# Kernel tuning notes

Hardware: AMD Instinct MI355X
Metric: run time of the kernel (lower is better)

## Reference

```python
import jax, jax.numpy as jnp
import numpy as np

ALPHA = 1.5
BETA = 45.0
LAMDA = 0.5
B = 8192   # batch_size
D = 128    # feature dim (hardcoded in original via zeros((1,128)))
V = 4      # number of views stacked in fj
EPS = 1e-12  # F.normalize eps


def _l2norm_rows(x):
    n = jnp.sqrt(jnp.sum(x * x, axis=-1, keepdims=True))
    return x / jnp.maximum(n, EPS)


def setup_inputs() -> dict:
    key = jax.random.key(0)
    k1, k2 = jax.random.split(key)
    fi = jax.random.normal(k1, (B, D), dtype=jnp.float32)
    fj = jax.random.normal(k2, (V, B, D), dtype=jnp.float32)
    # L2-normalize embeddings so exp(beta*(SVM - lamda)) stays finite (beta=45)
    fi = _l2norm_rows(fi)
    fj = _l2norm_rows(fj)
    return {"fi": fi, "fj": fj, "b": V}


def avg_svm(fi, fj):
    # Original: per-row softmax-weighted average of fj rows, renormalized,
    # dotted with fi row, averaged over the batch.
    A = fi @ fj.T                      # [B, B] pairwise logits
    W = jax.nn.softmax(A, axis=1)      # softmax over j (alphalist / sumofalpha)
    Vw = W @ fj                        # [B, D] softmax-weighted averages
    Vn = _l2norm_rows(Vw)              # F.normalize(p=2, dim=1)
    return jnp.mean(jnp.sum(fi * Vn, axis=1))  # mean_i fi[i] . Vn[i]


def reference(fi, fj, b):
    b = int(b)
    # SMM1 is recomputed identically every outer iteration in the original;
    # compute once and multiply the per-iteration term by (b-1).
    smm1 = avg_svm(fi, fi)
    if b > 2:
        # inner loop: SMM2sum is a running (cumulative) sum over j=1..b-2,
        # and exp(beta*(SMM2sum - lamda)) is added at every step.
        s_vals = jnp.stack([avg_svm(fi, fj[j]) for j in range(1, b - 1)])
        cum = jnp.cumsum(s_vals)
        ssum = jnp.sum(jnp.exp(BETA * (cum - LAMDA)))
    else:
        ssum = jnp.exp(BETA * (avg_svm(fi, fj) - LAMDA))
    term = (1.0 / ALPHA) * jnp.log1p(jnp.exp(-ALPHA * (smm1 - LAMDA))) \
         + (1.0 / BETA) * jnp.log1p(ssum)
    loss = (b - 1) * term
    return jnp.squeeze(loss)
```

## Files before the change

kernel.cpp:

```cpp
#include <hip/hip_runtime.h>

#define BDIM 8192
#define DDIM 128

typedef __attribute__((ext_vector_type(4))) float floatx4;
typedef __attribute__((ext_vector_type(4))) int   intx4;
typedef __attribute__((ext_vector_type(8))) int   intx8;
typedef long i64;

#define SLAB (BDIM * DDIM)
#define G8_OFF 64
#define G8T_OFF (64 + 3 * SLAB)

__device__ inline void load_lds16(const void* g, void* l) {
    __builtin_amdgcn_global_load_lds(
        (const __attribute__((address_space(1))) unsigned int*)g,
        (__attribute__((address_space(3))) unsigned int*)l, 16, 0, 0);
}

__device__ inline intx8 ld_pair(const char* base, int c0) {
    union { intx8 v; intx4 h[2]; } u;
    u.h[0] = *(const intx4*)(base + c0 * 16);
    u.h[1] = *(const intx4*)(base + (c0 ^ 1) * 16);
    return u.v;
}

__device__ inline float exp_fast(float x) {
    return __builtin_amdgcn_exp2f(x * 1.44269504088896341f);
}

__global__ __launch_bounds__(256)
void prep_kernel(const float* __restrict__ fi, const float* __restrict__ fj,
                 unsigned char* __restrict__ g8, unsigned char* __restrict__ g8T,
                 float* __restrict__ acc)
{
    const int p = blockIdx.y;
    const int kblock = blockIdx.x;
    const int rbase = kblock * 32;
    const int tid = threadIdx.x;
    if (p == 0 && kblock == 0 && tid < 8) acc[tid] = 0.f;
    const float* src = (p == 0) ? fi : (fj + (size_t)p * SLAB);

    __shared__ __align__(16) unsigned char T8[32][144];

    {
        const int row = tid >> 3, c = tid & 7;
        const float* sp = src + (size_t)(rbase + row) * DDIM + c * 16;
        float4 f0 = ((const float4*)sp)[0];
        float4 f1 = ((const float4*)sp)[1];
        float4 f2 = ((const float4*)sp)[2];
        float4 f3 = ((const float4*)sp)[3];
        alignas(16) int w[4];
        w[0] = __builtin_amdgcn_cvt_pk_fp8_f32(f0.x, f0.y, 0, false);
        w[0] = __builtin_amdgcn_cvt_pk_fp8_f32(f0.z, f0.w, w[0], true);
        w[1] = __builtin_amdgcn_cvt_pk_fp8_f32(f1.x, f1.y, 0, false);
        w[1] = __builtin_amdgcn_cvt_pk_fp8_f32(f1.z, f1.w, w[1], true);
        w[2] = __builtin_amdgcn_cvt_pk_fp8_f32(f2.x, f2.y, 0, false);
        w[2] = __builtin_amdgcn_cvt_pk_fp8_f32(f2.z, f2.w, w[2], true);
        w[3] = __builtin_amdgcn_cvt_pk_fp8_f32(f3.x, f3.y, 0, false);
        w[3] = __builtin_amdgcn_cvt_pk_fp8_f32(f3.z, f3.w, w[3], true);
        int4 v = *(int4*)w;
        *(int4*)(g8 + (size_t)p * SLAB + (size_t)(rbase + row) * DDIM + c * 16) = v;
        *(int4*)(&T8[row][c * 16]) = v;
    }
    __syncthreads();
    {
        const int d = tid >> 1, half = tid & 1;
        const int s = (d >> 2) & 3;
        alignas(16) unsigned char bb[16];
        #pragma unroll
        for (int x = 0; x < 16; ++x) {
            int g  = (half << 1) + (x >> 3);
            int u  = x & 7;
            int kl = ((g ^ s) << 2) + (u & 3) + ((u >> 2) << 4);
            bb[x] = T8[kl][d];
        }
        *(int4*)(g8T + (size_t)p * SLAB + (size_t)kblock * 4096 + d * 32 + half * 16) =
            *(int4*)bb;
    }
}

__global__ __launch_bounds__(256, 3)
void flash_kernel(const float* __restrict__ fi,
                  const unsigned char* __restrict__ g8,
                  const unsigned char* __restrict__ g8T,
                  float* __restrict__ acc)
{
    const int b = blockIdx.x;
    const int gp = (b & 7) * 96 + (b >> 3);
    const int p = gp >> 8;
    const int qbase = (gp & 255) * 32;
    const int tid = threadIdx.x;
    const int wave = tid >> 6, lane = tid & 63;
    const int quad = lane >> 4, col = lane & 15;

    __shared__ __align__(16) char smem[49792];
    #define KOFF 0
    #define VOFF 16384
    #define OOFF 32768
    #define PVOFF 49664

    const unsigned char* g8p  = g8  + (size_t)p * SLAB;
    const unsigned char* g8Tp = g8T + (size_t)p * SLAB;

    intx8 qf[2];
    #pragma unroll
    for (int qt = 0; qt < 2; ++qt) {
        const intx4* qp = (const intx4*)(g8 + (size_t)(qbase + qt * 16 + col) * DDIM +
                                         quad * 32);
        union { intx8 v; intx4 h[2]; } u;
        u.h[0] = qp[0];
        u.h[1] = qp[1];
        qf[qt] = u.v;
    }

    floatx4 O[2][8];
    #pragma unroll
    for (int qt = 0; qt < 2; ++qt)
        #pragma unroll
        for (int dt = 0; dt < 8; ++dt)
            O[qt][dt] = (floatx4){0.f, 0.f, 0.f, 0.f};

    const unsigned char* kSrc = g8p + (size_t)wave * 4096 +
        (size_t)(lane >> 3) * 128 + (size_t)(((lane & 7) ^ ((lane >> 3) & 7)) * 16);
    const unsigned char* vSrc = g8Tp + (size_t)wave * 4096 + (size_t)lane * 16;

    auto stage = [&]() {
        #pragma unroll
        for (int i = 0; i < 4; ++i)
            load_lds16(kSrc + i * 1024, smem + KOFF + wave * 4096 + i * 1024);
        #pragma unroll
        for (int i = 0; i < 4; ++i)
            load_lds16(vSrc + i * 1024, smem + VOFF + wave * 4096 + i * 1024);
        kSrc += 16384;
        vSrc += 16384;
    };

    const char* kb0 = smem + KOFF + wave * 4096 + col * 128;
    const char* kb1 = smem + KOFF + wave * 4096 + (16 + col) * 128;
    const int   kc  = (quad * 2) ^ (col & 7);
    const char* vbase = smem + VOFF + wave * 4096 + col * 32 +
                        ((quad ^ (col >> 2)) * 8);

    stage();

    for (int k = 0; k < 64; ++k) {
        asm volatile("s_waitcnt vmcnt(0)" ::: "memory");

        intx8 kf0 = ld_pair(kb0, kc);
        intx8 kf1 = ld_pair(kb1, kc);
        i64 vf[8];
        #pragma unroll
        for (int dt = 0; dt < 8; ++dt)
            vf[dt] = *(const i64*)(vbase + dt * 512);

        asm volatile("s_waitcnt lgkmcnt(0)" ::: "memory");
        if (k < 63) stage();

        floatx4 S[2][2];
        __builtin_amdgcn_s_setprio(1);
        S[0][0] = __builtin_amdgcn_mfma_scale_f32_16x16x128_f8f6f4(
            kf0, qf[0], (floatx4){0.f,0.f,0.f,0.f}, 0, 0, 0, 127, 0, 127);
        S[0][1] = __builtin_amdgcn_mfma_scale_f32_16x16x128_f8f6f4(
            kf0, qf[1], (floatx4){0.f,0.f,0.f,0.f}, 0, 0, 0, 127, 0, 127);
        S[1][0] = __builtin_amdgcn_mfma_scale_f32_16x16x128_f8f6f4(
            kf1, qf[0], (floatx4){0.f,0.f,0.f,0.f}, 0, 0, 0, 127, 0, 127);
        S[1][1] = __builtin_amdgcn_mfma_scale_f32_16x16x128_f8f6f4(
            kf1, qf[1], (floatx4){0.f,0.f,0.f,0.f}, 0, 0, 0, 127, 0, 127);
        __builtin_amdgcn_s_setprio(0);

        i64 pf[2];
        #pragma unroll
        for (int qt = 0; qt < 2; ++qt) {
            int w0 = __builtin_amdgcn_cvt_pk_fp8_f32(
                exp_fast(S[0][qt][0]), exp_fast(S[0][qt][1]), 0, false);
            w0 = __builtin_amdgcn_cvt_pk_fp8_f32(
                exp_fast(S[0][qt][2]), exp_fast(S[0][qt][3]), w0, true);
            int w1 = __builtin_amdgcn_cvt_pk_fp8_f32(
                exp_fast(S[1][qt][0]), exp_fast(S[1][qt][1]), 0, false);
            w1 = __builtin_amdgcn_cvt_pk_fp8_f32(
                exp_fast(S[1][qt][2]), exp_fast(S[1][qt][3]), w1, true);
            union { i64 l; int i[2]; } u;
            u.i[0] = w0;
            u.i[1] = w1;
            pf[qt] = u.l;
        }

        __builtin_amdgcn_s_setprio(1);
        #pragma unroll
        for (int qt = 0; qt < 2; ++qt)
            #pragma unroll
            for (int dt = 0; dt < 8; ++dt)
                O[qt][dt] = __builtin_amdgcn_mfma_f32_16x16x32_fp8_fp8(
                    pf[qt], vf[dt], O[qt][dt], 0, 0, 0);
        __builtin_amdgcn_s_setprio(0);
    }

    float* OL = (float*)(smem + OOFF);
    #pragma unroll 1
    for (int w = 0; w < 4; ++w) {
        if (wave == w) {
            #pragma unroll
            for (int qt = 0; qt < 2; ++qt)
                #pragma unroll
                for (int dt = 0; dt < 8; ++dt)
                    #pragma unroll
                    for (int r = 0; r < 4; ++r) {
                        const int q = qt * 16 + quad * 4 + r;
                        const int d = dt * 16 + col;
                        if (w == 0) OL[q * 132 + d]  = O[qt][dt][r];
                        else        OL[q * 132 + d] += O[qt][dt][r];
                    }
        }
        __syncthreads();
    }

    {
        const int q = tid >> 3, dc = (tid & 7) * 16;
        const float* fq = fi + (size_t)(qbase + q) * DDIM + dc;
        float dot = 0.f, nr = 0.f;
        #pragma unroll
        for (int u = 0; u < 16; ++u) {
            float o = OL[q * 132 + dc + u];
            dot += fq[u] * o;
            nr  += o * o;
        }
        #pragma unroll
        for (int m = 1; m < 8; m <<= 1) {
            dot += __shfl_xor(dot, m, 64);
            nr  += __shfl_xor(nr,  m, 64);
        }
        float* pv = (float*)(smem + PVOFF);
        if ((tid & 7) == 0)
            pv[q] = dot * rsqrtf(fmaxf(nr, 1e-30f));
        __syncthreads();
        if (tid < 32) {
            float val = pv[tid];
            #pragma unroll
            for (int m = 1; m < 32; m <<= 1) val += __shfl_xor(val, m, 64);
            if (tid == 0) atomicAdd(&acc[p], val);
        }
    }
}

__global__ void final_kernel(const float* __restrict__ acc, float* __restrict__ out)
{
    if (threadIdx.x == 0 && blockIdx.x == 0) {
        const double s0 = (double)acc[0] / (double)BDIM;
        const double s1 = (double)acc[1] / (double)BDIM;
        const double s2 = (double)acc[2] / (double)BDIM;
        const double t1 = (1.0 / 1.5) * log1p(exp(-1.5 * (s0 - 0.5)));
        const double ssum = exp(45.0 * (s1 - 0.5)) + exp(45.0 * (s1 + s2 - 0.5));
        const double t2 = (1.0 / 45.0) * log1p(ssum);
        out[0] = (float)(3.0 * (t1 + t2));
    }
}

extern "C" void kernel_launch(void* const* d_in, const int* in_sizes, int n_in,
                              void* d_out, int out_size, void* d_ws, size_t ws_size,
                              hipStream_t stream)
{
    const float* fi = (const float*)d_in[0];
    const float* fj = (const float*)d_in[1];

    float* acc = (float*)d_ws;
    unsigned char* g8  = (unsigned char*)d_ws + G8_OFF;
    unsigned char* g8T = (unsigned char*)d_ws + G8T_OFF;

    prep_kernel <<<dim3(BDIM / 32, 3), 256, 0, stream>>>(fi, fj, g8, g8T, acc);
    flash_kernel<<<dim3(768), 256, 0, stream>>>(fi, g8, g8T, acc);
    final_kernel<<<1, 64, 0, stream>>>(acc, (float*)d_out);
}
```

Measured before the change: 155.1 us.

## Batch four K tiles per PV step with K=128 fp8 MFMA and direct-global V loads

The PV product now accumulates P fragments from four consecutive key tiles into one 128-wide operand and issues the 16x16x128 scaled fp8 MFMA, cutting the PV MFMA count fourfold. V is read straight from global memory in a new transposed layout produced by the prep kernel, instead of being staged through LDS. This shrinks LDS use so more blocks can fit per CU. The cost is exposed global-load latency on the V fragments, which are no longer prefetched, and a different ordering of the transposed V data.

```diff
diff --git a/kernel.cpp b/kernel.cpp
--- a/kernel.cpp
+++ b/kernel.cpp
@@ -65,18 +65,23 @@
     }
     __syncthreads();
     {
-        const int d = tid >> 1, half = tid & 1;
-        const int s = (d >> 2) & 3;
-        alignas(16) unsigned char bb[16];
-        #pragma unroll
-        for (int x = 0; x < 16; ++x) {
-            int g  = (half << 1) + (x >> 3);
-            int u  = x & 7;
-            int kl = ((g ^ s) << 2) + (u & 3) + ((u >> 2) << 4);
-            bb[x] = T8[kl][d];
-        }
-        *(int4*)(g8T + (size_t)p * SLAB + (size_t)kblock * 4096 + d * 32 + half * 16) =
-            *(int4*)bb;
+        const int blk512 = kblock >> 4;
+        const int t      = (kblock >> 2) & 3;
+        const int wv     = kblock & 3;
+        unsigned char* dst = g8T + (size_t)p * SLAB + (size_t)blk512 * 65536 +
+                             (size_t)wv * 16384 + (size_t)t * 8;
+        const int d = tid >> 1;
+        #pragma unroll
+        for (int qi = 0; qi < 2; ++qi) {
+            const int quad = (tid & 1) * 2 + qi;
+            alignas(8) unsigned char bb[8];
+            #pragma unroll
+            for (int bq = 0; bq < 8; ++bq) {
+                int kl = quad * 4 + (bq & 3) + 16 * (bq >> 2);
+                bb[bq] = T8[kl][d];
+            }
+            *(i64*)(dst + (size_t)d * 128 + quad * 32) = *(i64*)bb;
+        }
     }
 }
 
@@ -94,11 +99,10 @@
     const int wave = tid >> 6, lane = tid & 63;
     const int quad = lane >> 4, col = lane & 15;
 
-    __shared__ __align__(16) char smem[49792];
+    __shared__ __align__(16) char smem[17408];
     #define KOFF 0
-    #define VOFF 16384
-    #define OOFF 32768
-    #define PVOFF 49664
+    #define OOFF 0
+    #define PVOFF 16896
 
     const unsigned char* g8p  = g8  + (size_t)p * SLAB;
     const unsigned char* g8Tp = g8T + (size_t)p * SLAB;
@@ -123,79 +127,116 @@
 
     const unsigned char* kSrc = g8p + (size_t)wave * 4096 +
         (size_t)(lane >> 3) * 128 + (size_t)(((lane & 7) ^ ((lane >> 3) & 7)) * 16);
-    const unsigned char* vSrc = g8Tp + (size_t)wave * 4096 + (size_t)lane * 16;
-
-    auto stage = [&]() {
+
+    auto stageK = [&]() {
         #pragma unroll
         for (int i = 0; i < 4; ++i)
             load_lds16(kSrc + i * 1024, smem + KOFF + wave * 4096 + i * 1024);
-        #pragma unroll
-        for (int i = 0; i < 4; ++i)
-            load_lds16(vSrc + i * 1024, smem + VOFF + wave * 4096 + i * 1024);
         kSrc += 16384;
-        vSrc += 16384;
     };
 
     const char* kb0 = smem + KOFF + wave * 4096 + col * 128;
     const char* kb1 = smem + KOFF + wave * 4096 + (16 + col) * 128;
     const int   kc  = (quad * 2) ^ (col & 7);
-    const char* vbase = smem + VOFF + wave * 4096 + col * 32 +
-                        ((quad ^ (col >> 2)) * 8);
-
-    stage();
-
-    for (int k = 0; k < 64; ++k) {
-        asm volatile("s_waitcnt vmcnt(0)" ::: "memory");
-
-        intx8 kf0 = ld_pair(kb0, kc);
-        intx8 kf1 = ld_pair(kb1, kc);
-        i64 vf[8];
-        #pragma unroll
-        for (int dt = 0; dt < 8; ++dt)
-            vf[dt] = *(const i64*)(vbase + dt * 512);
-
-        asm volatile("s_waitcnt lgkmcnt(0)" ::: "memory");
-        if (k < 63) stage();
-
-        floatx4 S[2][2];
-        __builtin_amdgcn_s_setprio(1);
-        S[0][0] = __builtin_amdgcn_mfma_scale_f32_16x16x128_f8f6f4(
-            kf0, qf[0], (floatx4){0.f,0.f,0.f,0.f}, 0, 0, 0, 127, 0, 127);
-        S[0][1] = __builtin_amdgcn_mfma_scale_f32_16x16x128_f8f6f4(
-            kf0, qf[1], (floatx4){0.f,0.f,0.f,0.f}, 0, 0, 0, 127, 0, 127);
-        S[1][0] = __builtin_amdgcn_mfma_scale_f32_16x16x128_f8f6f4(
-            kf1, qf[0], (floatx4){0.f,0.f,0.f,0.f}, 0, 0, 0, 127, 0, 127);
-        S[1][1] = __builtin_amdgcn_mfma_scale_f32_16x16x128_f8f6f4(
-            kf1, qf[1], (floatx4){0.f,0.f,0.f,0.f}, 0, 0, 0, 127, 0, 127);
-        __builtin_amdgcn_s_setprio(0);
-
-        i64 pf[2];
-        #pragma unroll
-        for (int qt = 0; qt < 2; ++qt) {
-            int w0 = __builtin_amdgcn_cvt_pk_fp8_f32(
-                exp_fast(S[0][qt][0]), exp_fast(S[0][qt][1]), 0, false);
-            w0 = __builtin_amdgcn_cvt_pk_fp8_f32(
-                exp_fast(S[0][qt][2]), exp_fast(S[0][qt][3]), w0, true);
-            int w1 = __builtin_amdgcn_cvt_pk_fp8_f32(
-                exp_fast(S[1][qt][0]), exp_fast(S[1][qt][1]), 0, false);
-            w1 = __builtin_amdgcn_cvt_pk_fp8_f32(
-                exp_fast(S[1][qt][2]), exp_fast(S[1][qt][3]), w1, true);
-            union { i64 l; int i[2]; } u;
-            u.i[0] = w0;
-            u.i[1] = w1;
-            pf[qt] = u.l;
-        }
-
-        __builtin_amdgcn_s_setprio(1);
-        #pragma unroll
-        for (int qt = 0; qt < 2; ++qt)
+
+    const unsigned char* gV = g8Tp + (size_t)wave * 16384 +
+                              (size_t)col * 128 + (size_t)quad * 32;
+
+    stageK();
+
+    #pragma unroll 1
+    for (int o = 0; o < 16; ++o) {
+        intx8 pa[2];
+
+        #pragma unroll
+        for (int t = 0; t < 4; ++t) {
+            const int g = o * 4 + t;
+            asm volatile("s_waitcnt vmcnt(0)" ::: "memory");
+
+            intx8 kf0 = ld_pair(kb0, kc);
+            intx8 kf1 = ld_pair(kb1, kc);
+            asm volatile("s_waitcnt lgkmcnt(0)" ::: "memory");
+            if (g < 63) stageK();
+
+            floatx4 S[2][2];
+            __builtin_amdgcn_s_setprio(1);
+            S[0][0] = __builtin_amdgcn_mfma_scale_f32_16x16x128_f8f6f4(
+                kf0, qf[0], (floatx4){0.f,0.f,0.f,0.f}, 0, 0, 0, 127, 0, 127);
+            S[0][1] = __builtin_amdgcn_mfma_scale_f32_16x16x128_f8f6f4(
+                kf0, qf[1], (floatx4){0.f,0.f,0.f,0.f}, 0, 0, 0, 127, 0, 127);
+            S[1][0] = __builtin_amdgcn_mfma_scale_f32_16x16x128_f8f6f4(
+                kf1, qf[0], (floatx4){0.f,0.f,0.f,0.f}, 0, 0, 0, 127, 0, 127);
+            S[1][1] = __builtin_amdgcn_mfma_scale_f32_16x16x128_f8f6f4(
+                kf1, qf[1], (floatx4){0.f,0.f,0.f,0.f}, 0, 0, 0, 127, 0, 127);
+            __builtin_amdgcn_s_setprio(0);
+
             #pragma unroll
-            for (int dt = 0; dt < 8; ++dt)
-                O[qt][dt] = __builtin_amdgcn_mfma_f32_16x16x32_fp8_fp8(
-                    pf[qt], vf[dt], O[qt][dt], 0, 0, 0);
-        __builtin_amdgcn_s_setprio(0);
-    }
-
+            for (int qt = 0; qt < 2; ++qt) {
+                int w0 = __builtin_amdgcn_cvt_pk_fp8_f32(
+                    exp_fast(S[0][qt][0]), exp_fast(S[0][qt][1]), 0, false);
+                w0 = __builtin_amdgcn_cvt_pk_fp8_f32(
+                    exp_fast(S[0][qt][2]), exp_fast(S[0][qt][3]), w0, true);
+                int w1 = __builtin_amdgcn_cvt_pk_fp8_f32(
+                    exp_fast(S[1][qt][0]), exp_fast(S[1][qt][1]), 0, false);
+                w1 = __builtin_amdgcn_cvt_pk_fp8_f32(
+                    exp_fast(S[1][qt][2]), exp_fast(S[1][qt][3]), w1, true);
+                pa[qt][2 * t]     = w0;
+                pa[qt][2 * t + 1] = w1;
+            }
+        }
+
+        const unsigned char* vb = gV + (size_t)o * 65536;
+        {
+            intx8 vf0 = *(const intx8*)(vb);
+            intx8 vf1 = *(const intx8*)(vb + 2048);
+            intx8 vf2 = *(const intx8*)(vb + 4096);
+            intx8 vf3 = *(const intx8*)(vb + 6144);
+            __builtin_amdgcn_s_setprio(1);
+            O[0][0] = __builtin_amdgcn_mfma_scale_f32_16x16x128_f8f6f4(
+                pa[0], vf0, O[0][0], 0, 0, 0, 127, 0, 127);
+            O[1][0] = __builtin_amdgcn_mfma_scale_f32_16x16x128_f8f6f4(
+                pa[1], vf0, O[1][0], 0, 0, 0, 127, 0, 127);
+            O[0][1] = __builtin_amdgcn_mfma_scale_f32_16x16x128_f8f6f4(
+                pa[0], vf1, O[0][1], 0, 0, 0, 127, 0, 127);
+            O[1][1] = __builtin_amdgcn_mfma_scale_f32_16x16x128_f8f6f4(
+                pa[1], vf1, O[1][1], 0, 0, 0, 127, 0, 127);
+            O[0][2] = __builtin_amdgcn_mfma_scale_f32_16x16x128_f8f6f4(
+                pa[0], vf2, O[0][2], 0, 0, 0, 127, 0, 127);
+            O[1][2] = __builtin_amdgcn_mfma_scale_f32_16x16x128_f8f6f4(
+                pa[1], vf2, O[1][2], 0, 0, 0, 127, 0, 127);
+            O[0][3] = __builtin_amdgcn_mfma_scale_f32_16x16x128_f8f6f4(
+                pa[0], vf3, O[0][3], 0, 0, 0, 127, 0, 127);
+            O[1][3] = __builtin_amdgcn_mfma_scale_f32_16x16x128_f8f6f4(
+                pa[1], vf3, O[1][3], 0, 0, 0, 127, 0, 127);
+            __builtin_amdgcn_s_setprio(0);
+        }
+        {
+            intx8 vf4 = *(const intx8*)(vb + 8192);
+            intx8 vf5 = *(const intx8*)(vb + 10240);
+            intx8 vf6 = *(const intx8*)(vb + 12288);
+            intx8 vf7 = *(const intx8*)(vb + 14336);
+            __builtin_amdgcn_s_setprio(1);
+            O[0][4] = __builtin_amdgcn_mfma_scale_f32_16x16x128_f8f6f4(
+                pa[0], vf4, O[0][4], 0, 0, 0, 127, 0, 127);
+            O[1][4] = __builtin_amdgcn_mfma_scale_f32_16x16x128_f8f6f4(
+                pa[1], vf4, O[1][4], 0, 0, 0, 127, 0, 127);
+            O[0][5] = __builtin_amdgcn_mfma_scale_f32_16x16x128_f8f6f4(
+                pa[0], vf5, O[0][5], 0, 0, 0, 127, 0, 127);
+            O[1][5] = __builtin_amdgcn_mfma_scale_f32_16x16x128_f8f6f4(
+                pa[1], vf5, O[1][5], 0, 0, 0, 127, 0, 127);
+            O[0][6] = __builtin_amdgcn_mfma_scale_f32_16x16x128_f8f6f4(
+                pa[0], vf6, O[0][6], 0, 0, 0, 127, 0, 127);
+            O[1][6] = __builtin_amdgcn_mfma_scale_f32_16x16x128_f8f6f4(
+                pa[1], vf6, O[1][6], 0, 0, 0, 127, 0, 127);
+            O[0][7] = __builtin_amdgcn_mfma_scale_f32_16x16x128_f8f6f4(
+                pa[0], vf7, O[0][7], 0, 0, 0, 127, 0, 127);
+            O[1][7] = __builtin_amdgcn_mfma_scale_f32_16x16x128_f8f6f4(
+                pa[1], vf7, O[1][7], 0, 0, 0, 127, 0, 127);
+            __builtin_amdgcn_s_setprio(0);
+        }
+    }
+
+    __syncthreads();
     float* OL = (float*)(smem + OOFF);
     #pragma unroll 1
     for (int w = 0; w < 4; ++w) {
```

Measured after the change: 219.4 us. 1.41x slower.

## Double-buffer K tiles in LDS and split K/V staging for deeper prefetch

Applied to the files above, without the earlier changes.

K tiles now alternate between two LDS buffers, so the next K tile is prefetched before the current one is consumed. The main loop waits with partial vmcnt/lgkmcnt counts instead of draining everything. V staging is moved after the exp/convert phase so its load overlaps the PV MFMAs. The last iteration is peeled, and the output reduction area now reuses the K region, which shrinks total LDS. The tighter fine-grained waitcnt assumptions risk race conditions if the counts do not match the real instruction ordering.

```diff
diff --git a/kernel.cpp b/kernel.cpp
--- a/kernel.cpp
+++ b/kernel.cpp
@@ -94,11 +94,11 @@
     const int wave = tid >> 6, lane = tid & 63;
     const int quad = lane >> 4, col = lane & 15;
 
-    __shared__ __align__(16) char smem[49792];
+    __shared__ __align__(16) char smem[49152];
     #define KOFF 0
-    #define VOFF 16384
-    #define OOFF 32768
-    #define PVOFF 49664
+    #define VOFF 32768
+    #define OOFF 0
+    #define PVOFF 16896
 
     const unsigned char* g8p  = g8  + (size_t)p * SLAB;
     const unsigned char* g8Tp = g8T + (size_t)p * SLAB;
@@ -125,37 +125,41 @@
         (size_t)(lane >> 3) * 128 + (size_t)(((lane & 7) ^ ((lane >> 3) & 7)) * 16);
     const unsigned char* vSrc = g8Tp + (size_t)wave * 4096 + (size_t)lane * 16;
 
-    auto stage = [&]() {
+    auto stageK = [&](int par) {
         #pragma unroll
         for (int i = 0; i < 4; ++i)
-            load_lds16(kSrc + i * 1024, smem + KOFF + wave * 4096 + i * 1024);
+            load_lds16(kSrc + i * 1024,
+                       smem + KOFF + par * 16384 + wave * 4096 + i * 1024);
+        kSrc += 16384;
+    };
+    auto stageV = [&]() {
         #pragma unroll
         for (int i = 0; i < 4; ++i)
             load_lds16(vSrc + i * 1024, smem + VOFF + wave * 4096 + i * 1024);
-        kSrc += 16384;
         vSrc += 16384;
     };
 
-    const char* kb0 = smem + KOFF + wave * 4096 + col * 128;
-    const char* kb1 = smem + KOFF + wave * 4096 + (16 + col) * 128;
-    const int   kc  = (quad * 2) ^ (col & 7);
+    const char* kbw  = smem + KOFF + wave * 4096;
+    const int   kc   = (quad * 2) ^ (col & 7);
     const char* vbase = smem + VOFF + wave * 4096 + col * 32 +
                         ((quad ^ (col >> 2)) * 8);
 
-    stage();
-
-    for (int k = 0; k < 64; ++k) {
-        asm volatile("s_waitcnt vmcnt(0)" ::: "memory");
-
-        intx8 kf0 = ld_pair(kb0, kc);
-        intx8 kf1 = ld_pair(kb1, kc);
+    stageK(0);
+    stageV();
+
+    for (int k = 0; k < 63; ++k) {
+        stageK((k + 1) & 1);
+        asm volatile("s_waitcnt vmcnt(4)" ::: "memory");
+
+        const char* kb = kbw + ((k & 1) << 14);
+        intx8 kf0 = ld_pair(kb + col * 128, kc);
+        intx8 kf1 = ld_pair(kb + (16 + col) * 128, kc);
         i64 vf[8];
         #pragma unroll
         for (int dt = 0; dt < 8; ++dt)
             vf[dt] = *(const i64*)(vbase + dt * 512);
 
-        asm volatile("s_waitcnt lgkmcnt(0)" ::: "memory");
-        if (k < 63) stage();
+        asm volatile("s_waitcnt lgkmcnt(8)" ::: "memory");
 
         floatx4 S[2][2];
         __builtin_amdgcn_s_setprio(1);
@@ -186,6 +190,9 @@
             pf[qt] = u.l;
         }
 
+        asm volatile("s_waitcnt lgkmcnt(0)" ::: "memory");
+        stageV();
+
         __builtin_amdgcn_s_setprio(1);
         #pragma unroll
         for (int qt = 0; qt < 2; ++qt)
@@ -195,6 +202,55 @@
                     pf[qt], vf[dt], O[qt][dt], 0, 0, 0);
         __builtin_amdgcn_s_setprio(0);
     }
+
+    {
+        asm volatile("s_waitcnt vmcnt(0)" ::: "memory");
+        const char* kb = kbw + 16384;
+        intx8 kf0 = ld_pair(kb + col * 128, kc);
+        intx8 kf1 = ld_pair(kb + (16 + col) * 128, kc);
+        i64 vf[8];
+        #pragma unroll
+        for (int dt = 0; dt < 8; ++dt)
+            vf[dt] = *(const i64*)(vbase + dt * 512);
+        asm volatile("s_waitcnt lgkmcnt(0)" ::: "memory");
+
+        floatx4 S[2][2];
+        S[0][0] = __builtin_amdgcn_mfma_scale_f32_16x16x128_f8f6f4(
+            kf0, qf[0], (floatx4){0.f,0.f,0.f,0.f}, 0, 0, 0, 127, 0, 127);
+        S[0][1] = __builtin_amdgcn_mfma_scale_f32_16x16x128_f8f6f4(
+            kf0, qf[1], (floatx4){0.f,0.f,0.f,0.f}, 0, 0, 0, 127, 0, 127);
+        S[1][0] = __builtin_amdgcn_mfma_scale_f32_16x16x128_f8f6f4(
+            kf1, qf[0], (floatx4){0.f,0.f,0.f,0.f}, 0, 0, 0, 127, 0, 127);
+        S[1][1] = __builtin_amdgcn_mfma_scale_f32_16x16x128_f8f6f4(
+            kf1, qf[1], (floatx4){0.f,0.f,0.f,0.f}, 0, 0, 0, 127, 0, 127);
+
+        i64 pf[2];
+        #pragma unroll
+        for (int qt = 0; qt < 2; ++qt) {
+            int w0 = __builtin_amdgcn_cvt_pk_fp8_f32(
+                exp_fast(S[0][qt][0]), exp_fast(S[0][qt][1]), 0, false);
+            w0 = __builtin_amdgcn_cvt_pk_fp8_f32(
+                exp_fast(S[0][qt][2]), exp_fast(S[0][qt][3]), w0, true);
+            int w1 = __builtin_amdgcn_cvt_pk_fp8_f32(
+                exp_fast(S[1][qt][0]), exp_fast(S[1][qt][1]), 0, false);
+            w1 = __builtin_amdgcn_cvt_pk_fp8_f32(
+                exp_fast(S[1][qt][2]), exp_fast(S[1][qt][3]), w1, true);
+            union { i64 l; int i[2]; } u;
+            u.i[0] = w0;
+            u.i[1] = w1;
+            pf[qt] = u.l;
+        }
+
+        #pragma unroll
+        for (int qt = 0; qt < 2; ++qt)
+            #pragma unroll
+            for (int dt = 0; dt < 8; ++dt)
+                O[qt][dt] = __builtin_amdgcn_mfma_f32_16x16x32_fp8_fp8(
+                    pf[qt], vf[dt], O[qt][dt], 0, 0, 0);
+    }
+
+    asm volatile("s_waitcnt vmcnt(0)" ::: "memory");
+    __syncthreads();
 
     float* OL = (float*)(smem + OOFF);
     #pragma unroll 1
```

After: 157.9 us. No clear change (+1.8%).
